# Kernel optimization log

Hardware: AMD Instinct MI355X
Metric: run time of the kernel (lower is better)

Reference implementation:

```python
import jax, jax.numpy as jnp
import numpy as np

N = 50000   # nodes
E = 1000000 # edges
D = 64      # hidden/filter channels
G = 5       # num_gaussians (edge_attr dim, unused by math)
N_CONV = 2


def setup_inputs() -> dict:
    key = jax.random.key(0)
    ks = jax.random.split(key, 8)
    x = jax.random.normal(ks[0], (N, D), dtype=jnp.float32)
    edge_index = jax.random.randint(ks[1], (2, E), 0, N)
    edge_weight = jax.random.uniform(ks[2], (E,), dtype=jnp.float32)
    edge_attr = jax.random.normal(ks[3], (E, G), dtype=jnp.float32)
    s = 1.0 / np.sqrt(D)
    lin0_w = jax.random.normal(ks[4], (D, D), dtype=jnp.float32) * s
    lin0_b = jnp.zeros((D,), dtype=jnp.float32)
    conv_w = jax.random.normal(ks[5], (N_CONV, D, D), dtype=jnp.float32) * s
    conv_b = jnp.zeros((N_CONV, D), dtype=jnp.float32)
    return dict(x=x, edge_index=edge_index, edge_weight=edge_weight,
                edge_attr=edge_attr, lin0_w=lin0_w, lin0_b=lin0_b,
                conv_w=conv_w, conv_b=conv_b)


def reference(x, edge_index, edge_weight, edge_attr, lin0_w, lin0_b, conv_w, conv_b):
    # edge_attr is accepted by the torch forward but never used by the convs.
    src, dst = edge_index[0], edge_index[1]
    # gcn_norm (no self loops): deg = scatter_add(w, dst); norm = d^-1/2[src]*w*d^-1/2[dst]
    deg = jax.ops.segment_sum(edge_weight, dst, num_segments=N)
    deg_safe = jnp.where(deg > 0, deg, 1.0)
    dinv = jnp.where(deg > 0, jax.lax.rsqrt(deg_safe), 0.0)
    norm = dinv[src] * edge_weight * dinv[dst]  # [E]

    out = jax.nn.relu(x @ lin0_w + lin0_b)  # lin0 + relu, [N, D]
    for i in range(N_CONV):
        h = out @ conv_w[i]                              # [N, D] transform
        msg = norm[:, None] * h[src]                     # gather + scale, [E, D]
        agg = jax.ops.segment_sum(msg, dst, num_segments=N)  # scatter-add, [N, D]
        out = out + jax.nn.relu(agg + conv_b[i])         # residual + relu
    return out
```

## Files before the change

### kernel.cpp

```cpp
#include <hip/hip_runtime.h>


#define TPB 256
#define BTPB 1024
#define EPT 8
#define EPB (BTPB * EPT)
#define CAP 64
#define MAXB 1024
#define BCAP 1536

__global__ void bin_edges_lds(const int* __restrict__ src, const int* __restrict__ dst,
                              const float* __restrict__ w, int* __restrict__ bcnt,
                              int2* __restrict__ bins, int E, int NB) {
    __shared__ int hist[MAXB];
    __shared__ int gb[MAXB];
    int t = threadIdx.x;
    for (int j = t; j < NB; j += BTPB) hist[j] = 0;
    __syncthreads();
    int base = blockIdx.x * EPB;
    int2 pk[EPT];
    int bk[EPT], lr[EPT];
#pragma unroll
    for (int i = 0; i < EPT; ++i) {
        int e = base + i * BTPB + t;
        bk[i] = -1;
        if (e < E) {
            int d = dst[e];
            int b = d >> 6;
            bk[i] = b;
            pk[i] = make_int2(src[e] | ((d & 63) << 26), __float_as_int(w[e]));
            lr[i] = atomicAdd(&hist[b], 1);
        }
    }
    __syncthreads();
    for (int j = t; j < NB; j += BTPB) {
        int h = hist[j];
        gb[j] = h ? atomicAdd(&bcnt[j], h) : 0;
    }
    __syncthreads();
#pragma unroll
    for (int i = 0; i < EPT; ++i) {
        if (bk[i] >= 0) {
            int p = gb[bk[i]] + lr[i];
            if (p < BCAP) bins[(size_t)bk[i] * BCAP + p] = pk[i];
        }
    }
}

__global__ void build_rows(const int* __restrict__ bcnt, const int2* __restrict__ bins,
                           int2* __restrict__ esw, int* __restrict__ cnt,
                           float* __restrict__ dinv, int N) {
    __shared__ int cnt64[64];
    __shared__ float wsum[64];
    int b = blockIdx.x;
    int t = threadIdx.x;
    if (t < 64) { cnt64[t] = 0; wsum[t] = 0.f; }
    __syncthreads();
    int c = min(bcnt[b], BCAP);
    for (int k = t; k < c; k += TPB) {
        int2 pk = bins[(size_t)b * BCAP + k];
        int ls = (unsigned)pk.x >> 26;
        int s = pk.x & 0x03FFFFFF;
        int p = atomicAdd(&cnt64[ls], 1);
        atomicAdd(&wsum[ls], __int_as_float(pk.y));
        if (p < CAP)
            esw[((size_t)(b * 64 + ls)) * CAP + p] = make_int2(s, pk.y);
    }
    __syncthreads();
    if (t < 64) {
        int node = b * 64 + t;
        if (node < N) {
            cnt[node] = min(cnt64[t], CAP);
            float sw = wsum[t];
            dinv[node] = sw > 0.f ? rsqrtf(sw) : 0.f;
        }
    }
}

__device__ __forceinline__ ushort f32_to_bf16_rne(float f) {
    uint b = __float_as_uint(f);
    return (ushort)((b + 0x7FFFu + ((b >> 16) & 1u)) >> 16);
}

template <bool RELU, bool BIAS, bool BF16OUT>
__global__ void gemm64t(const float* __restrict__ A, const float* __restrict__ W,
                        const float* __restrict__ bias, void* __restrict__ Cv, int n) {
    __shared__ float sW[64][64];
    __shared__ float sA[32][64];
    int t = threadIdx.x;
    const float4* W4 = (const float4*)W;
    float4* sW4 = (float4*)(&sW[0][0]);
#pragma unroll
    for (int i = 0; i < 4; ++i) sW4[t + i * 256] = W4[t + i * 256];
    int node0 = blockIdx.x * 32;
#pragma unroll
    for (int i = 0; i < 2; ++i) {
        int idx = t + i * 256;
        int nd = idx >> 4, ps = idx & 15;
        float4 v = make_float4(0.f, 0.f, 0.f, 0.f);
        if (node0 + nd < n) v = ((const float4*)A)[(size_t)(node0 + nd) * 16 + ps];
        ((float4*)&sA[nd][0])[ps] = v;
    }
    __syncthreads();
    int jg = t & 15;
    int np = t >> 4;
    int n0 = np * 2, n1 = n0 + 1;
    float4 acc0, acc1;
    if (BIAS) { acc0 = ((const float4*)bias)[jg]; acc1 = acc0; }
    else { acc0 = make_float4(0.f, 0.f, 0.f, 0.f); acc1 = acc0; }
#pragma unroll 4
    for (int k = 0; k < 64; ++k) {
        float4 wv = ((float4*)&sW[k][0])[jg];
        float a0 = sA[n0][k], a1 = sA[n1][k];
        acc0.x = fmaf(a0, wv.x, acc0.x);
        acc0.y = fmaf(a0, wv.y, acc0.y);
        acc0.z = fmaf(a0, wv.z, acc0.z);
        acc0.w = fmaf(a0, wv.w, acc0.w);
        acc1.x = fmaf(a1, wv.x, acc1.x);
        acc1.y = fmaf(a1, wv.y, acc1.y);
        acc1.z = fmaf(a1, wv.z, acc1.z);
        acc1.w = fmaf(a1, wv.w, acc1.w);
    }
    if (RELU) {
        acc0.x = fmaxf(acc0.x, 0.f); acc0.y = fmaxf(acc0.y, 0.f);
        acc0.z = fmaxf(acc0.z, 0.f); acc0.w = fmaxf(acc0.w, 0.f);
        acc1.x = fmaxf(acc1.x, 0.f); acc1.y = fmaxf(acc1.y, 0.f);
        acc1.z = fmaxf(acc1.z, 0.f); acc1.w = fmaxf(acc1.w, 0.f);
    }
    int g0 = node0 + n0, g1 = node0 + n1;
    if constexpr (BF16OUT) {
        ushort4 u0 = make_ushort4(f32_to_bf16_rne(acc0.x), f32_to_bf16_rne(acc0.y),
                                  f32_to_bf16_rne(acc0.z), f32_to_bf16_rne(acc0.w));
        ushort4 u1 = make_ushort4(f32_to_bf16_rne(acc1.x), f32_to_bf16_rne(acc1.y),
                                  f32_to_bf16_rne(acc1.z), f32_to_bf16_rne(acc1.w));
        if (g0 < n) ((ushort4*)Cv)[((size_t)g0 * 64 + jg * 4) >> 2] = u0;
        if (g1 < n) ((ushort4*)Cv)[((size_t)g1 * 64 + jg * 4) >> 2] = u1;
    } else {
        if (g0 < n) ((float4*)Cv)[((size_t)g0 * 64 + jg * 4) >> 2] = acc0;
        if (g1 < n) ((float4*)Cv)[((size_t)g1 * 64 + jg * 4) >> 2] = acc1;
    }
}

template <bool FIRST>
__global__ void gather_conv2(const ushort* __restrict__ hb, const int* __restrict__ cnt,
                             int2* __restrict__ esw, const float* __restrict__ dinv,
                             const float* __restrict__ b, float* __restrict__ out, int n) {
    int wv = (blockIdx.x * TPB + threadIdx.x) >> 6;
    int lane = threadIdx.x & 63;
    int half = lane >> 5, sub = lane & 31;
    int node = wv * 2 + half;
    bool nvalid = node < n;
    int c = nvalid ? cnt[node] : 0;
    int cmax = max(c, __shfl_xor(c, 32));
    float dd = 0.f;
    if (FIRST && nvalid) dd = dinv[node];
    const uint* h32 = (const uint*)hb;
    float accx = 0.f, accy = 0.f;
    for (int base = 0; base < cmax; base += 32) {
        int idx = base + sub;
        bool v = idx < c;
        int2 pv = v ? esw[(size_t)node * CAP + idx] : make_int2(0, 0);
        float nm;
        if (FIRST) {
            nm = v ? dinv[pv.x] * __int_as_float(pv.y) * dd : 0.f;
            if (v) esw[(size_t)node * CAP + idx].y = __float_as_int(nm);
        } else {
            nm = __int_as_float(pv.y);
        }
        int m = min(cmax - base, 32);
        int j = 0;
        for (; j + 4 <= m; j += 4) {
            int s0 = __shfl(pv.x, j, 32);
            int s1 = __shfl(pv.x, j + 1, 32);
            int s2 = __shfl(pv.x, j + 2, 32);
            int s3 = __shfl(pv.x, j + 3, 32);
            float n0 = __shfl(nm, j, 32);
            float n1 = __shfl(nm, j + 1, 32);
            float n2 = __shfl(nm, j + 2, 32);
            float n3 = __shfl(nm, j + 3, 32);
            uint u0 = h32[(size_t)s0 * 32 + sub];
            uint u1 = h32[(size_t)s1 * 32 + sub];
            uint u2 = h32[(size_t)s2 * 32 + sub];
            uint u3 = h32[(size_t)s3 * 32 + sub];
            accx = fmaf(n0, __uint_as_float(u0 << 16), accx);
            accy = fmaf(n0, __uint_as_float(u0 & 0xFFFF0000u), accy);
            accx = fmaf(n1, __uint_as_float(u1 << 16), accx);
            accy = fmaf(n1, __uint_as_float(u1 & 0xFFFF0000u), accy);
            accx = fmaf(n2, __uint_as_float(u2 << 16), accx);
            accy = fmaf(n2, __uint_as_float(u2 & 0xFFFF0000u), accy);
            accx = fmaf(n3, __uint_as_float(u3 << 16), accx);
            accy = fmaf(n3, __uint_as_float(u3 & 0xFFFF0000u), accy);
        }
        for (; j < m; ++j) {
            int s = __shfl(pv.x, j, 32);
            float nv = __shfl(nm, j, 32);
            uint u = h32[(size_t)s * 32 + sub];
            accx = fmaf(nv, __uint_as_float(u << 16), accx);
            accy = fmaf(nv, __uint_as_float(u & 0xFFFF0000u), accy);
        }
    }
    if (nvalid) {
        float2 bb = ((const float2*)b)[sub];
        float2* o2 = (float2*)out + (size_t)node * 32 + sub;
        float2 ov = *o2;
        ov.x = ov.x + fmaxf(accx + bb.x, 0.f);
        ov.y = ov.y + fmaxf(accy + bb.y, 0.f);
        *o2 = ov;
    }
}

extern "C" void kernel_launch(void* const* d_in, const int* in_sizes, int n_in,
                              void* d_out, int out_size, void* d_ws, size_t ws_size,
                              hipStream_t stream) {
    const float* x      = (const float*)d_in[0];
    const int*   ei     = (const int*)d_in[1];
    const float* ew     = (const float*)d_in[2];
    const float* lin0_w = (const float*)d_in[4];
    const float* lin0_b = (const float*)d_in[5];
    const float* conv_w = (const float*)d_in[6];
    const float* conv_b = (const float*)d_in[7];

    const int N = in_sizes[0] / 64;
    const int E = in_sizes[2];
    const int* src = ei;
    const int* dst = ei + E;
    const int NB = (N + 63) >> 6;

    char* ws = (char*)d_ws;
    size_t off = 0;
    auto alloc = [&](size_t bytes) {
        void* p = ws + off;
        off += (bytes + 255) & ~(size_t)255;
        return p;
    };
    int*    bcnt = (int*)alloc((size_t)NB * 4);
    int*    cnt  = (int*)alloc((size_t)N * 4);
    float*  dinv = (float*)alloc((size_t)N * 4);
    int2*   bins = (int2*)alloc((size_t)NB * BCAP * 8);
    int2*   esw  = (int2*)alloc((size_t)NB * 64 * CAP * 8);
    ushort* hb   = (ushort*)alloc((size_t)N * 64 * 2);

    float* out = (float*)d_out;
    int nblk_bin = (E + EPB - 1) / EPB;
    int nblk_gemm = (N + 31) / 32;
    int nblk_gather = (N + 7) / 8;

    hipMemsetAsync(bcnt, 0, (size_t)NB * 4, stream);
    bin_edges_lds<<<nblk_bin, BTPB, 0, stream>>>(src, dst, ew, bcnt, bins, E, NB);
    build_rows<<<NB, TPB, 0, stream>>>(bcnt, bins, esw, cnt, dinv, N);

    gemm64t<true, true, false><<<nblk_gemm, TPB, 0, stream>>>(x, lin0_w, lin0_b, out, N);

    gemm64t<false, false, true><<<nblk_gemm, TPB, 0, stream>>>(out, conv_w, nullptr, hb, N);
    gather_conv2<true><<<nblk_gather, TPB, 0, stream>>>(hb, cnt, esw, dinv, conv_b, out, N);

    gemm64t<false, false, true><<<nblk_gemm, TPB, 0, stream>>>(
        out, conv_w + (size_t)64 * 64, nullptr, hb, N);
    gather_conv2<false><<<nblk_gather, TPB, 0, stream>>>(hb, cnt, esw, dinv,
                                                         conv_b + 64, out, N);
}
```

Before: 121.7 us.

## Fuse lin0 with first conv transform and gather four nodes per wavefront

Merges the lin0+ReLU GEMM with the first conv weight GEMM into one kernel. The intermediate activation stays in LDS for the second product, so out no longer has to be re-read from global memory, and one launch disappears. The gather kernel now assigns 16 lanes per node (four nodes per wave) with 8-byte loads of four bf16 channels, instead of 32 lanes with 4-byte loads. That should improve per-lane memory-level parallelism but adds more divergence when neighbor counts within a wave differ. The fused kernel uses more LDS (two weight tiles plus two activation tiles), which may lower occupancy.

```diff
diff --git a/kernel.cpp b/kernel.cpp
--- a/kernel.cpp
+++ b/kernel.cpp
@@ -82,9 +82,78 @@
     return (ushort)((b + 0x7FFFu + ((b >> 16) & 1u)) >> 16);
 }
 
-template <bool RELU, bool BIAS, bool BF16OUT>
+__global__ void lin0_conv_fused(const float* __restrict__ x, const float* __restrict__ W0,
+                                const float* __restrict__ b0, const float* __restrict__ Wc,
+                                float* __restrict__ out, ushort* __restrict__ hb, int n) {
+    __shared__ float sW0[64][64];
+    __shared__ float sWc[64][64];
+    __shared__ float sA[32][64];
+    __shared__ float sO[32][64];
+    int t = threadIdx.x;
+    {
+        const float4* W04 = (const float4*)W0;
+        const float4* Wc4 = (const float4*)Wc;
+        float4* s0 = (float4*)(&sW0[0][0]);
+        float4* s1 = (float4*)(&sWc[0][0]);
+#pragma unroll
+        for (int i = 0; i < 4; ++i) {
+            s0[t + i * 256] = W04[t + i * 256];
+            s1[t + i * 256] = Wc4[t + i * 256];
+        }
+    }
+    int node0 = blockIdx.x * 32;
+#pragma unroll
+    for (int i = 0; i < 2; ++i) {
+        int idx = t + i * 256;
+        int nd = idx >> 4, ps = idx & 15;
+        float4 v = make_float4(0.f, 0.f, 0.f, 0.f);
+        if (node0 + nd < n) v = ((const float4*)x)[(size_t)(node0 + nd) * 16 + ps];
+        ((float4*)&sA[nd][0])[ps] = v;
+    }
+    __syncthreads();
+    int jg = t & 15;
+    int np = t >> 4;
+    int n0 = np * 2, n1 = n0 + 1;
+    float4 acc0 = ((const float4*)b0)[jg], acc1 = acc0;
+#pragma unroll 4
+    for (int k = 0; k < 64; ++k) {
+        float4 wv = ((float4*)&sW0[k][0])[jg];
+        float a0 = sA[n0][k], a1 = sA[n1][k];
+        acc0.x = fmaf(a0, wv.x, acc0.x); acc0.y = fmaf(a0, wv.y, acc0.y);
+        acc0.z = fmaf(a0, wv.z, acc0.z); acc0.w = fmaf(a0, wv.w, acc0.w);
+        acc1.x = fmaf(a1, wv.x, acc1.x); acc1.y = fmaf(a1, wv.y, acc1.y);
+        acc1.z = fmaf(a1, wv.z, acc1.z); acc1.w = fmaf(a1, wv.w, acc1.w);
+    }
+    acc0.x = fmaxf(acc0.x, 0.f); acc0.y = fmaxf(acc0.y, 0.f);
+    acc0.z = fmaxf(acc0.z, 0.f); acc0.w = fmaxf(acc0.w, 0.f);
+    acc1.x = fmaxf(acc1.x, 0.f); acc1.y = fmaxf(acc1.y, 0.f);
+    acc1.z = fmaxf(acc1.z, 0.f); acc1.w = fmaxf(acc1.w, 0.f);
+    ((float4*)&sO[n0][0])[jg] = acc0;
+    ((float4*)&sO[n1][0])[jg] = acc1;
+    int g0 = node0 + n0, g1 = node0 + n1;
+    if (g0 < n) ((float4*)out)[(size_t)g0 * 16 + jg] = acc0;
+    if (g1 < n) ((float4*)out)[(size_t)g1 * 16 + jg] = acc1;
+    __syncthreads();
+    float4 h0 = make_float4(0.f, 0.f, 0.f, 0.f), h1 = h0;
+#pragma unroll 4
+    for (int k = 0; k < 64; ++k) {
+        float4 wv = ((float4*)&sWc[k][0])[jg];
+        float a0 = sO[n0][k], a1 = sO[n1][k];
+        h0.x = fmaf(a0, wv.x, h0.x); h0.y = fmaf(a0, wv.y, h0.y);
+        h0.z = fmaf(a0, wv.z, h0.z); h0.w = fmaf(a0, wv.w, h0.w);
+        h1.x = fmaf(a1, wv.x, h1.x); h1.y = fmaf(a1, wv.y, h1.y);
+        h1.z = fmaf(a1, wv.z, h1.z); h1.w = fmaf(a1, wv.w, h1.w);
+    }
+    ushort4 u0 = make_ushort4(f32_to_bf16_rne(h0.x), f32_to_bf16_rne(h0.y),
+                              f32_to_bf16_rne(h0.z), f32_to_bf16_rne(h0.w));
+    ushort4 u1 = make_ushort4(f32_to_bf16_rne(h1.x), f32_to_bf16_rne(h1.y),
+                              f32_to_bf16_rne(h1.z), f32_to_bf16_rne(h1.w));
+    if (g0 < n) ((ushort4*)hb)[(size_t)g0 * 16 + jg] = u0;
+    if (g1 < n) ((ushort4*)hb)[(size_t)g1 * 16 + jg] = u1;
+}
+
 __global__ void gemm64t(const float* __restrict__ A, const float* __restrict__ W,
-                        const float* __restrict__ bias, void* __restrict__ Cv, int n) {
+                        ushort* __restrict__ C, int n) {
     __shared__ float sW[64][64];
     __shared__ float sA[32][64];
     int t = threadIdx.x;
@@ -105,58 +174,41 @@
     int jg = t & 15;
     int np = t >> 4;
     int n0 = np * 2, n1 = n0 + 1;
-    float4 acc0, acc1;
-    if (BIAS) { acc0 = ((const float4*)bias)[jg]; acc1 = acc0; }
-    else { acc0 = make_float4(0.f, 0.f, 0.f, 0.f); acc1 = acc0; }
+    float4 acc0 = make_float4(0.f, 0.f, 0.f, 0.f), acc1 = acc0;
 #pragma unroll 4
     for (int k = 0; k < 64; ++k) {
         float4 wv = ((float4*)&sW[k][0])[jg];
         float a0 = sA[n0][k], a1 = sA[n1][k];
-        acc0.x = fmaf(a0, wv.x, acc0.x);
-        acc0.y = fmaf(a0, wv.y, acc0.y);
-        acc0.z = fmaf(a0, wv.z, acc0.z);
-        acc0.w = fmaf(a0, wv.w, acc0.w);
-        acc1.x = fmaf(a1, wv.x, acc1.x);
-        acc1.y = fmaf(a1, wv.y, acc1.y);
-        acc1.z = fmaf(a1, wv.z, acc1.z);
-        acc1.w = fmaf(a1, wv.w, acc1.w);
-    }
-    if (RELU) {
-        acc0.x = fmaxf(acc0.x, 0.f); acc0.y = fmaxf(acc0.y, 0.f);
-        acc0.z = fmaxf(acc0.z, 0.f); acc0.w = fmaxf(acc0.w, 0.f);
-        acc1.x = fmaxf(acc1.x, 0.f); acc1.y = fmaxf(acc1.y, 0.f);
-        acc1.z = fmaxf(acc1.z, 0.f); acc1.w = fmaxf(acc1.w, 0.f);
+        acc0.x = fmaf(a0, wv.x, acc0.x); acc0.y = fmaf(a0, wv.y, acc0.y);
+        acc0.z = fmaf(a0, wv.z, acc0.z); acc0.w = fmaf(a0, wv.w, acc0.w);
+        acc1.x = fmaf(a1, wv.x, acc1.x); acc1.y = fmaf(a1, wv.y, acc1.y);
+        acc1.z = fmaf(a1, wv.z, acc1.z); acc1.w = fmaf(a1, wv.w, acc1.w);
     }
     int g0 = node0 + n0, g1 = node0 + n1;
-    if constexpr (BF16OUT) {
-        ushort4 u0 = make_ushort4(f32_to_bf16_rne(acc0.x), f32_to_bf16_rne(acc0.y),
-                                  f32_to_bf16_rne(acc0.z), f32_to_bf16_rne(acc0.w));
-        ushort4 u1 = make_ushort4(f32_to_bf16_rne(acc1.x), f32_to_bf16_rne(acc1.y),
-                                  f32_to_bf16_rne(acc1.z), f32_to_bf16_rne(acc1.w));
-        if (g0 < n) ((ushort4*)Cv)[((size_t)g0 * 64 + jg * 4) >> 2] = u0;
-        if (g1 < n) ((ushort4*)Cv)[((size_t)g1 * 64 + jg * 4) >> 2] = u1;
-    } else {
-        if (g0 < n) ((float4*)Cv)[((size_t)g0 * 64 + jg * 4) >> 2] = acc0;
-        if (g1 < n) ((float4*)Cv)[((size_t)g1 * 64 + jg * 4) >> 2] = acc1;
-    }
+    ushort4 u0 = make_ushort4(f32_to_bf16_rne(acc0.x), f32_to_bf16_rne(acc0.y),
+                              f32_to_bf16_rne(acc0.z), f32_to_bf16_rne(acc0.w));
+    ushort4 u1 = make_ushort4(f32_to_bf16_rne(acc1.x), f32_to_bf16_rne(acc1.y),
+                              f32_to_bf16_rne(acc1.z), f32_to_bf16_rne(acc1.w));
+    if (g0 < n) ((ushort4*)C)[(size_t)g0 * 16 + jg] = u0;
+    if (g1 < n) ((ushort4*)C)[(size_t)g1 * 16 + jg] = u1;
 }
 
 template <bool FIRST>
-__global__ void gather_conv2(const ushort* __restrict__ hb, const int* __restrict__ cnt,
+__global__ void gather_conv4(const ushort* __restrict__ hb, const int* __restrict__ cnt,
                              int2* __restrict__ esw, const float* __restrict__ dinv,
                              const float* __restrict__ b, float* __restrict__ out, int n) {
     int wv = (blockIdx.x * TPB + threadIdx.x) >> 6;
     int lane = threadIdx.x & 63;
-    int half = lane >> 5, sub = lane & 31;
-    int node = wv * 2 + half;
+    int q = lane >> 4, sub = lane & 15;
+    int node = wv * 4 + q;
     bool nvalid = node < n;
     int c = nvalid ? cnt[node] : 0;
-    int cmax = max(c, __shfl_xor(c, 32));
-    float dd = 0.f;
-    if (FIRST && nvalid) dd = dinv[node];
-    const uint* h32 = (const uint*)hb;
-    float accx = 0.f, accy = 0.f;
-    for (int base = 0; base < cmax; base += 32) {
+    int m1 = max(c, __shfl_xor(c, 16));
+    int cmax = max(m1, __shfl_xor(m1, 32));
+    float dd = (FIRST && nvalid) ? dinv[node] : 0.f;
+    const float2* h64 = (const float2*)hb;
+    float4 acc = make_float4(0.f, 0.f, 0.f, 0.f);
+    for (int base = 0; base < cmax; base += 16) {
         int idx = base + sub;
         bool v = idx < c;
         int2 pv = v ? esw[(size_t)node * CAP + idx] : make_int2(0, 0);
@@ -167,45 +219,63 @@
         } else {
             nm = __int_as_float(pv.y);
         }
-        int m = min(cmax - base, 32);
+        int m = min(cmax - base, 16);
         int j = 0;
         for (; j + 4 <= m; j += 4) {
-            int s0 = __shfl(pv.x, j, 32);
-            int s1 = __shfl(pv.x, j + 1, 32);
-            int s2 = __shfl(pv.x, j + 2, 32);
-            int s3 = __shfl(pv.x, j + 3, 32);
-            float n0 = __shfl(nm, j, 32);
-            float n1 = __shfl(nm, j + 1, 32);
-            float n2 = __shfl(nm, j + 2, 32);
-            float n3 = __shfl(nm, j + 3, 32);
-            uint u0 = h32[(size_t)s0 * 32 + sub];
-            uint u1 = h32[(size_t)s1 * 32 + sub];
-            uint u2 = h32[(size_t)s2 * 32 + sub];
-            uint u3 = h32[(size_t)s3 * 32 + sub];
-            accx = fmaf(n0, __uint_as_float(u0 << 16), accx);
-            accy = fmaf(n0, __uint_as_float(u0 & 0xFFFF0000u), accy);
-            accx = fmaf(n1, __uint_as_float(u1 << 16), accx);
-            accy = fmaf(n1, __uint_as_float(u1 & 0xFFFF0000u), accy);
-            accx = fmaf(n2, __uint_as_float(u2 << 16), accx);
-            accy = fmaf(n2, __uint_as_float(u2 & 0xFFFF0000u), accy);
-            accx = fmaf(n3, __uint_as_float(u3 << 16), accx);
-            accy = fmaf(n3, __uint_as_float(u3 & 0xFFFF0000u), accy);
+            int s0 = __shfl(pv.x, j, 16);
+            int s1 = __shfl(pv.x, j + 1, 16);
+            int s2 = __shfl(pv.x, j + 2, 16);
+            int s3 = __shfl(pv.x, j + 3, 16);
+            float n0 = __shfl(nm, j, 16);
+            float n1 = __shfl(nm, j + 1, 16);
+            float n2 = __shfl(nm, j + 2, 16);
+            float n3 = __shfl(nm, j + 3, 16);
+            float2 f0 = h64[(size_t)s0 * 16 + sub];
+            float2 f1 = h64[(size_t)s1 * 16 + sub];
+            float2 f2 = h64[(size_t)s2 * 16 + sub];
+            float2 f3 = h64[(size_t)s3 * 16 + sub];
+            uint a, bb;
+            a = __float_as_uint(f0.x); bb = __float_as_uint(f0.y);
+            acc.x = fmaf(n0, __uint_as_float(a << 16), acc.x);
+            acc.y = fmaf(n0, __uint_as_float(a & 0xFFFF0000u), acc.y);
+            acc.z = fmaf(n0, __uint_as_float(bb << 16), acc.z);
+            acc.w = fmaf(n0, __uint_as_float(bb & 0xFFFF0000u), acc.w);
+            a = __float_as_uint(f1.x); bb = __float_as_uint(f1.y);
+            acc.x = fmaf(n1, __uint_as_float(a << 16), acc.x);
+            acc.y = fmaf(n1, __uint_as_float(a & 0xFFFF0000u), acc.y);
+            acc.z = fmaf(n1, __uint_as_float(bb << 16), acc.z);
+            acc.w = fmaf(n1, __uint_as_float(bb & 0xFFFF0000u), acc.w);
+            a = __float_as_uint(f2.x); bb = __float_as_uint(f2.y);
+            acc.x = fmaf(n2, __uint_as_float(a << 16), acc.x);
+            acc.y = fmaf(n2, __uint_as_float(a & 0xFFFF0000u), acc.y);
+            acc.z = fmaf(n2, __uint_as_float(bb << 16), acc.z);
+            acc.w = fmaf(n2, __uint_as_float(bb & 0xFFFF0000u), acc.w);
+            a = __float_as_uint(f3.x); bb = __float_as_uint(f3.y);
+            acc.x = fmaf(n3, __uint_as_float(a << 16), acc.x);
+            acc.y = fmaf(n3, __uint_as_float(a & 0xFFFF0000u), acc.y);
+            acc.z = fmaf(n3, __uint_as_float(bb << 16), acc.z);
+            acc.w = fmaf(n3, __uint_as_float(bb & 0xFFFF0000u), acc.w);
         }
         for (; j < m; ++j) {
-            int s = __shfl(pv.x, j, 32);
-            float nv = __shfl(nm, j, 32);
-            uint u = h32[(size_t)s * 32 + sub];
-            accx = fmaf(nv, __uint_as_float(u << 16), accx);
-            accy = fmaf(nv, __uint_as_float(u & 0xFFFF0000u), accy);
+            int s = __shfl(pv.x, j, 16);
+            float nv = __shfl(nm, j, 16);
+            float2 f = h64[(size_t)s * 16 + sub];
+            uint a = __float_as_uint(f.x), bb = __float_as_uint(f.y);
+            acc.x = fmaf(nv, __uint_as_float(a << 16), acc.x);
+            acc.y = fmaf(nv, __uint_as_float(a & 0xFFFF0000u), acc.y);
+            acc.z = fmaf(nv, __uint_as_float(bb << 16), acc.z);
+            acc.w = fmaf(nv, __uint_as_float(bb & 0xFFFF0000u), acc.w);
         }
     }
     if (nvalid) {
-        float2 bb = ((const float2*)b)[sub];
-        float2* o2 = (float2*)out + (size_t)node * 32 + sub;
-        float2 ov = *o2;
-        ov.x = ov.x + fmaxf(accx + bb.x, 0.f);
-        ov.y = ov.y + fmaxf(accy + bb.y, 0.f);
-        *o2 = ov;
+        float4 bv = ((const float4*)b)[sub];
+        float4* o4 = (float4*)out + (size_t)node * 16 + sub;
+        float4 ov = *o4;
+        ov.x = ov.x + fmaxf(acc.x + bv.x, 0.f);
+        ov.y = ov.y + fmaxf(acc.y + bv.y, 0.f);
+        ov.z = ov.z + fmaxf(acc.z + bv.z, 0.f);
+        ov.w = ov.w + fmaxf(acc.w + bv.w, 0.f);
+        *o4 = ov;
     }
 }
 
@@ -243,19 +313,16 @@
     float* out = (float*)d_out;
     int nblk_bin = (E + EPB - 1) / EPB;
     int nblk_gemm = (N + 31) / 32;
-    int nblk_gather = (N + 7) / 8;
+    int nblk_gather = (N + 15) / 16;
 
     hipMemsetAsync(bcnt, 0, (size_t)NB * 4, stream);
     bin_edges_lds<<<nblk_bin, BTPB, 0, stream>>>(src, dst, ew, bcnt, bins, E, NB);
     build_rows<<<NB, TPB, 0, stream>>>(bcnt, bins, esw, cnt, dinv, N);
 
-    gemm64t<true, true, false><<<nblk_gemm, TPB, 0, stream>>>(x, lin0_w, lin0_b, out, N);
-
-    gemm64t<false, false, true><<<nblk_gemm, TPB, 0, stream>>>(out, conv_w, nullptr, hb, N);
-    gather_conv2<true><<<nblk_gather, TPB, 0, stream>>>(hb, cnt, esw, dinv, conv_b, out, N);
-
-    gemm64t<false, false, true><<<nblk_gemm, TPB, 0, stream>>>(
-        out, conv_w + (size_t)64 * 64, nullptr, hb, N);
-    gather_conv2<false><<<nblk_gather, TPB, 0, stream>>>(hb, cnt, esw, dinv,
+    lin0_conv_fused<<<nblk_gemm, TPB, 0, stream>>>(x, lin0_w, lin0_b, conv_w, out, hb, N);
+    gather_conv4<true><<<nblk_gather, TPB, 0, stream>>>(hb, cnt, esw, dinv, conv_b, out, N);
+
+    gemm64t<<<nblk_gemm, TPB, 0, stream>>>(out, conv_w + (size_t)64 * 64, hb, N);
+    gather_conv4<false><<<nblk_gather, TPB, 0, stream>>>(hb, cnt, esw, dinv,
                                                          conv_b + 64, out, N);
 }
```

Measured after the change: 116.7 us. 4.1% less time.
